# Optimization experiments

Measured on AMD Instinct MI355X. Metric: run time of the kernel, lower is better.

## Reference

```python
import jax, jax.numpy as jnp
import numpy as np

B, C, H, W = 4, 64, 128, 128
NUM_HEAD = 1
SCALE = (C // NUM_HEAD) ** (-0.5)


def setup_inputs():
    key = jax.random.key(0)
    ks = jax.random.split(key, 32)
    def nrm(k, shape, s=0.05):
        return jax.random.normal(k, shape, jnp.float32) * s
    inp = {"x": jax.random.normal(ks[0], (B, C, H, W), jnp.float32)}
    i = 1
    for wn, bn in [("Wq", "bq"), ("Wk", "bk"), ("Wv", "bv"), ("Wl", "bl"), ("Wo", "bo"), ("Wp", "bp")]:
        inp[wn] = nrm(ks[i], (C, C)); i += 1
        inp[bn] = nrm(ks[i], (C,)); i += 1
    inp["sch_dw"] = nrm(ks[i], (C, 1, 5, 1)); i += 1
    inp["sch_dwb"] = nrm(ks[i], (C,)); i += 1
    inp["sch_pw"] = nrm(ks[i], (C, C, 1, 1)); i += 1
    inp["sch_pwb"] = nrm(ks[i], (C,)); i += 1
    inp["scv_dw"] = nrm(ks[i], (C, 1, 1, 5)); i += 1
    inp["scv_dwb"] = nrm(ks[i], (C,)); i += 1
    inp["scv_pw"] = nrm(ks[i], (C, C, 1, 1)); i += 1
    inp["scv_pwb"] = nrm(ks[i], (C,)); i += 1
    inp["convh_w"] = nrm(ks[i], (C, C, 1, 1)); i += 1
    inp["convh_b"] = nrm(ks[i], (C,)); i += 1
    inp["dsc_dw"] = nrm(ks[i], (C, 1, 3, 3)); i += 1
    inp["dsc_dwb"] = nrm(ks[i], (C,)); i += 1
    inp["dsc_pw"] = nrm(ks[i], (C, C, 1, 1)); i += 1
    inp["dsc_pwb"] = nrm(ks[i], (C,)); i += 1
    inp["ln_g"] = jnp.ones((C,), jnp.float32)
    inp["ln_b"] = jnp.zeros((C,), jnp.float32)
    return inp


def _linear(x, w, b):  # x [B,N,C], w [C,C] (torch Linear convention: y = x @ w.T + b)
    return x @ w.T + b


def _dwconv(x, w, b, pad):  # depthwise: x [B,C,H,W], w [C,1,kh,kw]
    y = jax.lax.conv_general_dilated(x, w, (1, 1), [(pad[0], pad[0]), (pad[1], pad[1])],
                                     dimension_numbers=("NCHW", "OIHW", "NCHW"),
                                     feature_group_count=x.shape[1])
    return y + b[None, :, None, None]


def _pwconv(x, w, b):  # 1x1 conv: w [Co,Ci,1,1]
    return jnp.einsum("bchw,oc->bohw", x, w[:, :, 0, 0]) + b[None, :, None, None]


def _attn(q, k, v):  # [B,N,C] each; dense NxN softmax attention
    a = jax.nn.softmax(jnp.einsum("bnc,bmc->bnm", q, k) * SCALE, axis=-1)
    return jnp.einsum("bnm,bmc->bnc", a, v)


def _up2_bilinear(x):  # bilinear, scale 2, align_corners=True
    Bb, Cc, Hh, Ww = x.shape
    def coords(n):
        s = jnp.linspace(0.0, n - 1.0, 2 * n)
        i0 = jnp.floor(s).astype(jnp.int32)
        i1 = jnp.minimum(i0 + 1, n - 1)
        return i0, i1, (s - i0).astype(x.dtype)
    y0, y1, wy = coords(Hh)
    x0, x1, wx = coords(Ww)
    r = x[:, :, y0, :] * (1.0 - wy)[None, None, :, None] + x[:, :, y1, :] * wy[None, None, :, None]
    return r[:, :, :, x0] * (1.0 - wx) + r[:, :, :, x1] * wx


def _forward(x, Wq, bq, Wk, bk, Wv, bv, Wl, bl, Wo, bo, Wp, bp,
             sch_dw, sch_dwb, sch_pw, sch_pwb, scv_dw, scv_dwb, scv_pw, scv_pwb,
             convh_w, convh_b, dsc_dw, dsc_dwb, dsc_pw, dsc_pwb, ln_g, ln_b):
    Bb, Cc, Hh, Ww = x.shape
    # AvgPool2d(2,2)
    xp = x.reshape(Bb, Cc, Hh // 2, 2, Ww // 2, 2).mean((3, 5))
    Hp, Wp_ = Hh // 2, Ww // 2
    N = Hp * Wp_
    # forward_lpg: GAP-gated self-attention producing low-freq prompt
    gap = xp.mean((2, 3), keepdims=True)
    xg = (gap * xp).reshape(Bb, Cc, N).transpose(0, 2, 1)  # [B,N,C]
    q = _linear(xg, Wq, bq); k = _linear(xg, Wk, bk); v = _linear(xg, Wv, bv)
    prompt_l = _linear(_attn(q, k, v), Wl, bl).transpose(0, 2, 1).reshape(Bb, Cc, Hp, Wp_)
    # forward_hpg: separable strip-conv branches -> high-freq prompt
    x_h = _pwconv(jax.nn.gelu(_dwconv(xp, sch_dw, sch_dwb, (2, 0)), approximate=False), sch_pw, sch_pwb)
    x_v = _pwconv(jax.nn.gelu(_dwconv(xp, scv_dw, scv_dwb, (0, 2)), approximate=False), scv_pw, scv_pwb)
    prompt_h = _pwconv(x_h + x_v, convh_w, convh_b)
    # forward_pgc: cross-attention Q=high, K=low, V=linear(x)
    x_V = _linear(xp.reshape(Bb, Cc, N).transpose(0, 2, 1), Wo, bo)
    x_K = prompt_l.reshape(Bb, Cc, N).transpose(0, 2, 1)
    x_Q = prompt_h.reshape(Bb, Cc, N).transpose(0, 2, 1)
    prompt = _attn(x_Q, x_K, x_V)
    prompt = _linear(prompt, Wp, bp) + x_V
    # LayerNorm over channel dim
    mu = prompt.mean(-1, keepdims=True)
    var = jnp.mean((prompt - mu) ** 2, axis=-1, keepdims=True)
    p_norm = (prompt - mu) / jnp.sqrt(var + 1e-5) * ln_g + ln_b
    p_norm = p_norm.transpose(0, 2, 1).reshape(Bb, Cc, Hp, Wp_)
    # dsc: depthwise 3x3 -> GELU -> 1x1, residual
    out = _pwconv(jax.nn.gelu(_dwconv(p_norm, dsc_dw, dsc_dwb, (1, 1)), approximate=False), dsc_pw, dsc_pwb) + p_norm
    return _up2_bilinear(out)


def reference(x, Wq, bq, Wk, bk, Wv, bv, Wl, bl, Wo, bo, Wp, bp,
              sch_dw, sch_dwb, sch_pw, sch_pwb, scv_dw, scv_dwb, scv_pw, scv_pwb,
              convh_w, convh_b, dsc_dw, dsc_dwb, dsc_pw, dsc_pwb, ln_g, ln_b):
    return _forward(x, Wq, bq, Wk, bk, Wv, bv, Wl, bl, Wo, bo, Wp, bp,
                    sch_dw, sch_dwb, sch_pw, sch_pwb, scv_dw, scv_dwb, scv_pw, scv_pwb,
                    convh_w, convh_b, dsc_dw, dsc_dwb, dsc_pw, dsc_pwb, ln_g, ln_b)
```

## Files before the change

### kernel.cpp

```cpp
#include <hip/hip_runtime.h>
#include <math.h>

#define Bn 4
#define Cn 64
#define Np 4096
#define NSPLIT 4
#define SCALE2 0.18033688011112042f

typedef unsigned short ushort_t;
typedef __attribute__((ext_vector_type(4))) float f32x4;
typedef __attribute__((ext_vector_type(8))) short bf16x8;
typedef __attribute__((ext_vector_type(4))) short bf16x4;

__device__ __forceinline__ float gelu_exact(float x) {
    return 0.5f * x * (1.0f + erff(x * 0.70710678118654752440f));
}
__device__ __forceinline__ ushort_t f2bf(float f) {
    unsigned int u = __float_as_uint(f);
    u += 0x7fffu + ((u >> 16) & 1u);
    return (ushort_t)(u >> 16);
}
__device__ __forceinline__ ushort_t f2bf_tr(float f) {
    return (ushort_t)(__float_as_uint(f) >> 16);
}
__device__ __forceinline__ float bf2f(ushort_t h) {
    return __uint_as_float(((unsigned int)h) << 16);
}
__device__ __forceinline__ void gload_lds16(const ushort_t* g, ushort_t* l) {
    __builtin_amdgcn_global_load_lds(
        (const __attribute__((address_space(1))) void*)g,
        (__attribute__((address_space(3))) void*)l, 16, 0, 0);
}
__device__ __forceinline__ bf16x8 cvt8(const float v[8]) {
    bf16x8 r;
    #pragma unroll
    for (int j = 0; j < 8; ++j) r[j] = (short)f2bf(v[j]);
    return r;
}
__device__ __forceinline__ void gemm16(const bf16x8 af[2], const float* __restrict__ W,
                                       int l16, int quad, f32x4* acc) {
    #pragma unroll
    for (int cb = 0; cb < 4; ++cb) {
        #pragma unroll
        for (int ks = 0; ks < 2; ++ks) {
            const float* p = W + (cb * 16 + l16) * 64 + ks * 32 + quad * 8;
            float v[8];
            #pragma unroll
            for (int j = 0; j < 8; ++j) v[j] = p[j];
            acc[cb] = __builtin_amdgcn_mfma_f32_16x16x32_bf16(af[ks], cvt8(v), acc[cb], 0, 0, 0);
        }
    }
}
__device__ __forceinline__ void gemm16T(const bf16x8 af[2], const float* __restrict__ W,
                                        int l16, int quad, f32x4* acc) {
    #pragma unroll
    for (int cb = 0; cb < 4; ++cb) {
        #pragma unroll
        for (int ks = 0; ks < 2; ++ks) {
            const float* p = W + (cb * 16 + l16) * 64 + ks * 32 + quad * 8;
            float v[8];
            #pragma unroll
            for (int j = 0; j < 8; ++j) v[j] = p[j];
            acc[cb] = __builtin_amdgcn_mfma_f32_16x16x32_bf16(cvt8(v), af[ks], acc[cb], 0, 0, 0);
        }
    }
}
__device__ __forceinline__ void aload(const float* xs, int row, int quad, bf16x8 af[2]) {
    #pragma unroll
    for (int ks = 0; ks < 2; ++ks) {
        float v[8];
        #pragma unroll
        for (int j = 0; j < 8; ++j) v[j] = xs[(ks * 32 + quad * 8 + j) * 65 + row];
        af[ks] = cvt8(v);
    }
}
__device__ __forceinline__ void stage_bchw(const float* __restrict__ X, int b, int n0, int t,
                                           float* xs) {
    #pragma unroll
    for (int u = 0; u < 16; ++u) {
        int idx = t + u * 256;
        int c = idx >> 6, nl = idx & 63;
        xs[c * 65 + nl] = X[((size_t)(b * Cn + c)) * Np + n0 + nl];
    }
}
__device__ __forceinline__ void stage_comb(const ushort_t* __restrict__ OpB, const float* linv,
                                           int b, int n0, int t, float* xs) {
    const size_t SS = (size_t)Bn * Np * Cn;
    #pragma unroll
    for (int u = 0; u < 16; ++u) {
        int idx = t + u * 256;
        int nl = idx >> 6, c = idx & 63;
        size_t gi = ((size_t)(b * Np + n0 + nl)) * Cn + c;
        float s = bf2f(OpB[gi]) + bf2f(OpB[SS + gi]) +
                  bf2f(OpB[2 * SS + gi]) + bf2f(OpB[3 * SS + gi]);
        xs[c * 65 + nl] = s * linv[nl];
    }
}
__device__ __forceinline__ void store_bnc_T(ushort_t* __restrict__ Y, int b, int n, int quad,
                                            const f32x4* acc, const float* __restrict__ bias,
                                            float mult) {
    #pragma unroll
    for (int cb = 0; cb < 4; ++cb) {
        int o0 = cb * 16 + quad * 4;
        ushort4 pk;
        pk.x = f2bf((acc[cb][0] + bias[o0 + 0]) * mult);
        pk.y = f2bf((acc[cb][1] + bias[o0 + 1]) * mult);
        pk.z = f2bf((acc[cb][2] + bias[o0 + 2]) * mult);
        pk.w = f2bf((acc[cb][3] + bias[o0 + 3]) * mult);
        *(ushort4*)(Y + ((size_t)(b * Np + n)) * Cn + o0) = pk;
    }
}
__device__ __forceinline__ void store_bchw_bf16(ushort_t* __restrict__ Y, int b, int nb, int l16,
                                                const f32x4* acc, const float* __restrict__ bias) {
    #pragma unroll
    for (int cb = 0; cb < 4; ++cb) {
        int col = cb * 16 + l16;
        float bb = bias[col];
        ushort4 pk;
        pk.x = f2bf(acc[cb][0] + bb); pk.y = f2bf(acc[cb][1] + bb);
        pk.z = f2bf(acc[cb][2] + bb); pk.w = f2bf(acc[cb][3] + bb);
        *(ushort4*)(Y + ((size_t)(b * Cn + col)) * Np + nb) = pk;
    }
}

__global__ void avgpool_kernel(const float* __restrict__ x, float* __restrict__ xp,
                               float* __restrict__ gap4k,
                               const float* __restrict__ convh_w, const float* __restrict__ convh_b,
                               const float* __restrict__ sch_pw, const float* __restrict__ sch_pwb,
                               const float* __restrict__ scv_pw, const float* __restrict__ scv_pwb,
                               float* __restrict__ Wc1, float* __restrict__ Wc2,
                               float* __restrict__ bcv) {
    if (blockIdx.x < 4096) {
        int idx = blockIdx.x * 256 + threadIdx.x;
        int j  = idx & 63;
        int i  = (idx >> 6) & 63;
        int bc = idx >> 12;
        const float* p = x + ((size_t)bc * 128 + 2 * i) * 128 + 2 * j;
        float v = 0.25f * (p[0] + p[1] + p[128] + p[129]);
        xp[idx] = v;
        float s = v;
        #pragma unroll
        for (int off = 1; off < 64; off <<= 1) s += __shfl_xor(s, off, 64);
        __shared__ float sm[4];
        if ((threadIdx.x & 63) == 0) sm[threadIdx.x >> 6] = s;
        __syncthreads();
        if (threadIdx.x == 0) gap4k[blockIdx.x] = sm[0] + sm[1] + sm[2] + sm[3];
    } else {
        int g = (blockIdx.x - 4096) * 256 + threadIdx.x;
        int sel = g >> 12, idx = g & 4095;
        int o = idx >> 6, c = idx & 63;
        const float* pw = sel ? scv_pw : sch_pw;
        float acc = 0.f;
        #pragma unroll 8
        for (int m = 0; m < 64; ++m) acc += convh_w[o * 64 + m] * pw[m * 64 + c];
        (sel ? Wc2 : Wc1)[idx] = acc * SCALE2;
        if (g < 64) {
            float ab = convh_b[g];
            for (int m = 0; m < 64; ++m) ab += convh_w[g * 64 + m] * (sch_pwb[m] + scv_pwb[m]);
            bcv[g] = ab * SCALE2;
        }
    }
}

__global__ __launch_bounds__(256) void qkv_dw_kernel(
    const float* __restrict__ xp, const float* __restrict__ gap4k,
    const float* __restrict__ Wq, const float* __restrict__ bq,
    const float* __restrict__ Wk, const float* __restrict__ bk,
    const float* __restrict__ Wv, const float* __restrict__ bv,
    const float* __restrict__ Wo, const float* __restrict__ bo,
    ushort_t* __restrict__ qb, ushort_t* __restrict__ kb, ushort_t* __restrict__ vb,
    float* __restrict__ xV, ushort_t* __restrict__ xVtb,
    const float* __restrict__ wv5, const float* __restrict__ bv5,
    const float* __restrict__ wh5, const float* __restrict__ bh5,
    ushort_t* __restrict__ gh, ushort_t* __restrict__ gv) {
    int b = blockIdx.y, t = threadIdx.x;
    if (blockIdx.x >= 64) {
        int part = blockIdx.x - 64;
        int e = part * 1024 + t * 4;
        size_t base = (size_t)b * (Cn * Np) + e;
        int c = e >> 12, i = (e >> 6) & 63, j = e & 63;
        const float* p = xp + ((size_t)(b * Cn + c)) * Np;
        float accV[4], accH[4];
        #pragma unroll
        for (int k = 0; k < 4; ++k) { accV[k] = bv5[c]; accH[k] = bh5[c]; }
        #pragma unroll
        for (int d = 0; d < 5; ++d) {
            int ii = i + d - 2;
            if (ii >= 0 && ii < 64) {
                #pragma unroll
                for (int k = 0; k < 4; ++k) accV[k] += wv5[c * 5 + d] * p[ii * 64 + j + k];
            }
        }
        #pragma unroll
        for (int k = 0; k < 4; ++k) {
            #pragma unroll
            for (int d = 0; d < 5; ++d) {
                int jj = j + k + d - 2;
                if (jj >= 0 && jj < 64) accH[k] += wh5[c * 5 + d] * p[i * 64 + jj];
            }
        }
        ushort4 ph, pv_;
        ph.x = f2bf(gelu_exact(accV[0])); ph.y = f2bf(gelu_exact(accV[1]));
        ph.z = f2bf(gelu_exact(accV[2])); ph.w = f2bf(gelu_exact(accV[3]));
        pv_.x = f2bf(gelu_exact(accH[0])); pv_.y = f2bf(gelu_exact(accH[1]));
        pv_.z = f2bf(gelu_exact(accH[2])); pv_.w = f2bf(gelu_exact(accH[3]));
        *(ushort4*)(gh + base) = ph;
        *(ushort4*)(gv + base) = pv_;
        return;
    }
    __shared__ float xs[64 * 65];
    __shared__ float gl[64];
    int n0 = blockIdx.x * 64;
    int wv_ = t >> 6, lane = t & 63, l16 = lane & 15, quad = lane >> 4;
    stage_bchw(xp, b, n0, t, xs);
    if (t < 64) {
        float s = 0.f;
        #pragma unroll
        for (int u = 0; u < 16; ++u) s += gap4k[(b * 64 + t) * 16 + u];
        gl[t] = s * (1.f / 4096.f);
    }
    __syncthreads();
    int row = wv_ * 16 + l16;
    int n   = n0 + wv_ * 16 + l16;
    int nb  = n0 + wv_ * 16 + quad * 4;
    bf16x8 ar[2], ag[2];
    #pragma unroll
    for (int ks = 0; ks < 2; ++ks) {
        float vr[8], vg[8];
        #pragma unroll
        for (int j = 0; j < 8; ++j) {
            int k = ks * 32 + quad * 8 + j;
            float xv = xs[k * 65 + row];
            vr[j] = xv; vg[j] = xv * gl[k];
        }
        ar[ks] = cvt8(vr); ag[ks] = cvt8(vg);
    }
    f32x4 acc[4];
    #pragma unroll
    for (int cb = 0; cb < 4; ++cb) acc[cb] = (f32x4){0.f, 0.f, 0.f, 0.f};
    gemm16T(ag, Wq, l16, quad, acc);
    store_bnc_T(qb, b, n, quad, acc, bq, SCALE2);
    #pragma unroll
    for (int cb = 0; cb < 4; ++cb) acc[cb] = (f32x4){0.f, 0.f, 0.f, 0.f};
    gemm16T(ag, Wk, l16, quad, acc);
    store_bnc_T(kb, b, n, quad, acc, bk, 1.f);
    #pragma unroll
    for (int cb = 0; cb < 4; ++cb) acc[cb] = (f32x4){0.f, 0.f, 0.f, 0.f};
    gemm16(ag, Wv, l16, quad, acc);
    store_bchw_bf16(vb, b, nb, l16, acc, bv);
    #pragma unroll
    for (int cb = 0; cb < 4; ++cb) acc[cb] = (f32x4){0.f, 0.f, 0.f, 0.f};
    gemm16(ar, Wo, l16, quad, acc);
    #pragma unroll
    for (int cb = 0; cb < 4; ++cb) {
        int col = cb * 16 + l16;
        float bb = bo[col];
        ushort4 pk;
        float y0 = acc[cb][0] + bb, y1 = acc[cb][1] + bb, y2 = acc[cb][2] + bb, y3 = acc[cb][3] + bb;
        xV[((size_t)(b * Np + nb + 0)) * Cn + col] = y0;
        xV[((size_t)(b * Np + nb + 1)) * Cn + col] = y1;
        xV[((size_t)(b * Np + nb + 2)) * Cn + col] = y2;
        xV[((size_t)(b * Np + nb + 3)) * Cn + col] = y3;
        pk.x = f2bf(y0); pk.y = f2bf(y1); pk.z = f2bf(y2); pk.w = f2bf(y3);
        *(ushort4*)(xVtb + ((size_t)(b * Cn + col)) * Np + nb) = pk;
    }
}

__device__ __forceinline__ void attn_body(
    int xblk, int b, const ushort_t* __restrict__ Qb, const ushort_t* __restrict__ Kb,
    const ushort_t* __restrict__ Vtb, ushort_t* __restrict__ OpB, float* __restrict__ Lpart,
    ushort_t* smem) {
    ushort_t* kt0 = smem;
    ushort_t* vt0 = smem + 8192;
    int split = xblk >> 6;
    int qt    = xblk & 63;
    int n0    = qt * 64;
    int t     = threadIdx.x;
    int wave  = t >> 6, lane = t & 63;
    int l16   = lane & 15, quad = lane >> 4;

    const ushort_t* qp = Qb + ((size_t)(b * Np) + n0 + wave * 16 + l16) * Cn + quad * 8;
    bf16x8 aq0 = *(const bf16x8*)(qp);
    bf16x8 aq1 = *(const bf16x8*)(qp + 32);

    f32x4 oa[4];
    float psum = 0.f;
    #pragma unroll
    for (int db = 0; db < 4; ++db) oa[db] = (f32x4){0.f, 0.f, 0.f, 0.f};

    int lrow = lane >> 3;
    int kvbase = split * (Np / NSPLIT);
    const ushort_t* Kg = Qb == nullptr ? nullptr : Kb + ((size_t)b * Np) * Cn;
    const ushort_t* Vg = Vtb + ((size_t)b * Cn) * Np;

    auto stage = [&](int buf, int k0) {
        int wh = wave & 1;
        if (wave < 2) {
            ushort_t* dst = kt0 + buf * 4096 + wh * 2048;
            #pragma unroll
            for (int u = 0; u < 4; ++u) {
                int r = wh * 32 + u * 8 + lrow;
                int jsw = ((lane & 7) ^ lrow ^ (wh * 4 + u)) & 7;
                gload_lds16(Kg + ((size_t)(k0 + r)) * Cn + jsw * 8, dst + u * 512);
            }
        } else {
            ushort_t* dst = vt0 + buf * 4096 + wh * 2048;
            #pragma unroll
            for (int u = 0; u < 4; ++u) {
                int d = wh * 32 + u * 8 + lrow;
                int jsw = ((lane & 7) ^ lrow ^ (wh * 4 + u)) & 7;
                gload_lds16(Vg + (size_t)d * Np + k0 + jsw * 8, dst + u * 512);
            }
        }
    };
    const int NT = (Np / NSPLIT) / 64;
    stage(0, kvbase);
    __syncthreads();

    for (int m = 0; m < NT; ++m) {
        int cur = m & 1;
        if (m + 1 < NT) stage(1 - cur, kvbase + (m + 1) * 64);
        const ushort_t* ktc = kt0 + cur * 4096;
        const ushort_t* vtc = vt0 + cur * 4096;

        f32x4 sa[4];
        #pragma unroll
        for (int cb = 0; cb < 4; ++cb) sa[cb] = (f32x4){0.f, 0.f, 0.f, 0.f};
        #pragma unroll
        for (int cb = 0; cb < 4; ++cb) {
            int key = ((l16 & 7) ^ (cb * 2 + (l16 >> 3))) & 7;
            const ushort_t* krow = ktc + (cb * 16 + l16) * 64;
            bf16x8 bk0 = *(const bf16x8*)(krow + ((quad    ) ^ key) * 8);
            bf16x8 bk1 = *(const bf16x8*)(krow + ((quad + 4) ^ key) * 8);
            sa[cb] = __builtin_amdgcn_mfma_f32_16x16x32_bf16(bk0, aq0, sa[cb], 0, 0, 0);
            sa[cb] = __builtin_amdgcn_mfma_f32_16x16x32_bf16(bk1, aq1, sa[cb], 0, 0, 0);
        }
        bf16x4 pb[4];
        #pragma unroll
        for (int cb = 0; cb < 4; ++cb) {
            float p0 = exp2f(sa[cb][0]), p1 = exp2f(sa[cb][1]);
            float p2 = exp2f(sa[cb][2]), p3 = exp2f(sa[cb][3]);
            psum += (p0 + p1) + (p2 + p3);
            bf16x4 pk;
            pk[0] = (short)f2bf_tr(p0); pk[1] = (short)f2bf_tr(p1);
            pk[2] = (short)f2bf_tr(p2); pk[3] = (short)f2bf_tr(p3);
            pb[cb] = pk;
        }
        #pragma unroll
        for (int kc = 0; kc < 4; ++kc) {
            #pragma unroll
            for (int db = 0; db < 4; ++db) {
                int d = db * 16 + l16;
                int key = ((l16 & 7) ^ (db * 2 + (l16 >> 3))) & 7;
                int phys = (kc * 2 + (quad >> 1)) ^ key;
                const ushort_t* va = vtc + d * 64 + phys * 8 + (quad & 1) * 4;
                bf16x4 av = *(const bf16x4*)va;
                oa[db] = __builtin_amdgcn_mfma_f32_16x16x16bf16_1k(av, pb[kc], oa[db], 0, 0, 0);
            }
        }
        __syncthreads();
    }
    psum += __shfl_xor(psum, 16, 64);
    psum += __shfl_xor(psum, 32, 64);
    size_t obase = ((size_t)(split * Bn + b)) * Np;
    int n = n0 + wave * 16 + l16;
    if (quad == 0) Lpart[obase + n] = psum;
    #pragma unroll
    for (int db = 0; db < 4; ++db) {
        ushort4 pk;
        pk.x = f2bf(oa[db][0]); pk.y = f2bf(oa[db][1]);
        pk.z = f2bf(oa[db][2]); pk.w = f2bf(oa[db][3]);
        *(ushort4*)(OpB + (obase + n) * Cn + db * 16 + quad * 4) = pk;
    }
}

__device__ __forceinline__ void hpg_body(
    int tile, int b, const ushort_t* __restrict__ gh, const ushort_t* __restrict__ gv,
    const float* __restrict__ Wc1, const float* __restrict__ Wc2, const float* __restrict__ bcv,
    ushort_t* __restrict__ xQb, ushort_t* smem) {
    ushort_t* xs1 = smem;
    ushort_t* xs2 = smem + 4608;
    int n0 = tile * 64, t = threadIdx.x;
    int wv_ = t >> 6, lane = t & 63, l16 = lane & 15, quad = lane >> 4;
    #pragma unroll
    for (int u = 0; u < 4; ++u) {
        int lin = u * 256 + t;
        int c = lin >> 4, nl4 = (lin & 15) * 4;
        size_t gi = ((size_t)(b * Cn + c)) * Np + n0 + nl4;
        ushort4 g1 = *(const ushort4*)(gh + gi);
        ushort4 g2 = *(const ushort4*)(gv + gi);
        xs1[(nl4 + 0) * 72 + c] = g1.x; xs1[(nl4 + 1) * 72 + c] = g1.y;
        xs1[(nl4 + 2) * 72 + c] = g1.z; xs1[(nl4 + 3) * 72 + c] = g1.w;
        xs2[(nl4 + 0) * 72 + c] = g2.x; xs2[(nl4 + 1) * 72 + c] = g2.y;
        xs2[(nl4 + 2) * 72 + c] = g2.z; xs2[(nl4 + 3) * 72 + c] = g2.w;
    }
    __syncthreads();
    int row = wv_ * 16 + l16;
    bf16x8 a1[2], a2[2];
    #pragma unroll
    for (int ks = 0; ks < 2; ++ks) {
        a1[ks] = *(const bf16x8*)(xs1 + row * 72 + ks * 32 + quad * 8);
        a2[ks] = *(const bf16x8*)(xs2 + row * 72 + ks * 32 + quad * 8);
    }
    f32x4 acc[4];
    #pragma unroll
    for (int cb = 0; cb < 4; ++cb) acc[cb] = (f32x4){0.f, 0.f, 0.f, 0.f};
    gemm16T(a1, Wc1, l16, quad, acc);
    gemm16T(a2, Wc2, l16, quad, acc);
    store_bnc_T(xQb, b, n0 + wv_ * 16 + l16, quad, acc, bcv, 1.f);
}

__global__ __launch_bounds__(256) void attn_hpg_kernel(
    const ushort_t* __restrict__ Qb, const ushort_t* __restrict__ Kb,
    const ushort_t* __restrict__ Vtb, ushort_t* __restrict__ OpB, float* __restrict__ Lpart,
    const ushort_t* __restrict__ gh, const ushort_t* __restrict__ gv,
    const float* __restrict__ Wc1, const float* __restrict__ Wc2,
    const float* __restrict__ bcv, ushort_t* __restrict__ xQb) {
    __shared__ ushort_t smem[16384];
    int b = blockIdx.y;
    if (blockIdx.x < 256)
        attn_body(blockIdx.x, b, Qb, Kb, Vtb, OpB, Lpart, smem);
    else
        hpg_body(blockIdx.x - 256, b, gh, gv, Wc1, Wc2, bcv, xQb, smem);
}

__global__ __launch_bounds__(256) void wl_mfma(
    const ushort_t* __restrict__ OpB, const float* __restrict__ Lp,
    const float* __restrict__ Wl, const float* __restrict__ bl, ushort_t* __restrict__ xKb) {
    __shared__ float xs[64 * 65];
    __shared__ float linv[64];
    int b = blockIdx.y, n0 = blockIdx.x * 64, t = threadIdx.x;
    int wv_ = t >> 6, lane = t & 63, l16 = lane & 15, quad = lane >> 4;
    if (t < 64) {
        size_t li = (size_t)b * Np + n0 + t;
        const size_t LS = (size_t)Bn * Np;
        linv[t] = 1.f / (Lp[li] + Lp[LS + li] + Lp[2 * LS + li] + Lp[3 * LS + li]);
    }
    __syncthreads();
    stage_comb(OpB, linv, b, n0, t, xs);
    __syncthreads();
    bf16x8 af[2];
    aload(xs, wv_ * 16 + l16, quad, af);
    f32x4 acc[4];
    #pragma unroll
    for (int cb = 0; cb < 4; ++cb) acc[cb] = (f32x4){0.f, 0.f, 0.f, 0.f};
    gemm16T(af, Wl, l16, quad, acc);
    store_bnc_T(xKb, b, n0 + wv_ * 16 + l16, quad, acc, bl, 1.f);
}

__global__ __launch_bounds__(256) void linln_mfma(
    const ushort_t* __restrict__ OpB, const float* __restrict__ Lp,
    const float* __restrict__ Wp, const float* __restrict__ bp,
    const float* __restrict__ xV, const float* __restrict__ g, const float* __restrict__ beta,
    float* __restrict__ out) {
    __shared__ float xs[64 * 65];
    __shared__ float linv[64];
    int b = blockIdx.y, n0 = blockIdx.x * 64, t = threadIdx.x;
    int wv_ = t >> 6, lane = t & 63, l16 = lane & 15, quad = lane >> 4;
    if (t < 64) {
        size_t li = (size_t)b * Np + n0 + t;
        const size_t LS = (size_t)Bn * Np;
        linv[t] = 1.f / (Lp[li] + Lp[LS + li] + Lp[2 * LS + li] + Lp[3 * LS + li]);
    }
    __syncthreads();
    stage_comb(OpB, linv, b, n0, t, xs);
    __syncthreads();
    bf16x8 af[2];
    aload(xs, wv_ * 16 + l16, quad, af);
    f32x4 acc[4];
    #pragma unroll
    for (int cb = 0; cb < 4; ++cb) acc[cb] = (f32x4){0.f, 0.f, 0.f, 0.f};
    gemm16(af, Wp, l16, quad, acc);
    int nb = n0 + wv_ * 16 + quad * 4;
    float vals[4][4], gc[4], bec[4];
    #pragma unroll
    for (int cb = 0; cb < 4; ++cb) {
        int col = cb * 16 + l16;
        float bb = bp[col];
        gc[cb] = g[col]; bec[cb] = beta[col];
        #pragma unroll
        for (int r = 0; r < 4; ++r)
            vals[cb][r] = acc[cb][r] + bb + xV[((size_t)(b * Np + nb + r)) * Cn + col];
    }
    f32x4 yn[4];
    #pragma unroll
    for (int r = 0; r < 4; ++r) {
        float s = 0.f, s2 = 0.f;
        #pragma unroll
        for (int cb = 0; cb < 4; ++cb) { s += vals[cb][r]; s2 += vals[cb][r] * vals[cb][r]; }
        #pragma unroll
        for (int off = 1; off < 16; off <<= 1) {
            s  += __shfl_xor(s, off, 64);
            s2 += __shfl_xor(s2, off, 64);
        }
        float mu  = s * (1.f / 64.f);
        float var = s2 * (1.f / 64.f) - mu * mu;
        float ivs = rsqrtf(var + 1e-5f);
        #pragma unroll
        for (int cb = 0; cb < 4; ++cb)
            yn[cb][r] = (vals[cb][r] - mu) * ivs * gc[cb] + bec[cb];
    }
    #pragma unroll
    for (int cb = 0; cb < 4; ++cb)
        *(f32x4*)(out + ((size_t)(b * Cn + cb * 16 + l16)) * Np + nb) = yn[cb];
}

__global__ void dw3x3_gelu_kernel(const float* __restrict__ xin, const float* __restrict__ w,
                                  const float* __restrict__ bias, float* __restrict__ out) {
    int idx = blockIdx.x * 256 + threadIdx.x;
    int j = idx & 63, i = (idx >> 6) & 63, bc = idx >> 12, c = bc & 63;
    const float* p = xin + (size_t)bc * Np;
    float acc = bias[c];
    #pragma unroll
    for (int dy = 0; dy < 3; ++dy) {
        int ii = i + dy - 1;
        if (ii < 0 || ii >= 64) continue;
        #pragma unroll
        for (int dx = 0; dx < 3; ++dx) {
            int jj = j + dx - 1;
            if (jj < 0 || jj >= 64) continue;
            acc += w[c * 9 + dy * 3 + dx] * p[ii * 64 + jj];
        }
    }
    out[idx] = gelu_exact(acc);
}

__global__ __launch_bounds__(256) void dsc_mfma(
    const float* __restrict__ X, const float* __restrict__ W, const float* __restrict__ bias,
    const float* __restrict__ res, float* __restrict__ out) {
    __shared__ float xs[64 * 65];
    int b = blockIdx.y, n0 = blockIdx.x * 64, t = threadIdx.x;
    int wv_ = t >> 6, lane = t & 63, l16 = lane & 15, quad = lane >> 4;
    stage_bchw(X, b, n0, t, xs);
    __syncthreads();
    bf16x8 af[2];
    aload(xs, wv_ * 16 + l16, quad, af);
    f32x4 acc[4];
    #pragma unroll
    for (int cb = 0; cb < 4; ++cb) acc[cb] = (f32x4){0.f, 0.f, 0.f, 0.f};
    gemm16(af, W, l16, quad, acc);
    int nb = n0 + wv_ * 16 + quad * 4;
    #pragma unroll
    for (int cb = 0; cb < 4; ++cb) {
        int col = cb * 16 + l16;
        float bb = bias[col];
        size_t oi = ((size_t)(b * Cn + col)) * Np + nb;
        f32x4 rv = *(const f32x4*)(res + oi);
        f32x4 v4;
        #pragma unroll
        for (int r = 0; r < 4; ++r) v4[r] = acc[cb][r] + bb + rv[r];
        *(f32x4*)(out + oi) = v4;
    }
}

__global__ void upsample_kernel(const float* __restrict__ in, float* __restrict__ out) {
    int idx = blockIdx.x * 256 + threadIdx.x;
    int x  = idx & 127;
    int y  = (idx >> 7) & 127;
    int bc = idx >> 14;
    float sy = y * (63.f / 127.f);
    float sx = x * (63.f / 127.f);
    int y0 = (int)sy, x0 = (int)sx;
    float fy = sy - y0, fx = sx - x0;
    int y1 = min(y0 + 1, 63), x1 = min(x0 + 1, 63);
    const float* p = in + (size_t)bc * Np;
    float v00 = p[y0 * 64 + x0], v01 = p[y0 * 64 + x1];
    float v10 = p[y1 * 64 + x0], v11 = p[y1 * 64 + x1];
    out[idx] = (v00 * (1.f - fx) + v01 * fx) * (1.f - fy) +
               (v10 * (1.f - fx) + v11 * fx) * fy;
}

extern "C" void kernel_launch(void* const* d_in, const int* in_sizes, int n_in,
                              void* d_out, int out_size, void* d_ws, size_t ws_size,
                              hipStream_t stream) {
    const float* x       = (const float*)d_in[0];
    const float* Wq      = (const float*)d_in[1];
    const float* bq      = (const float*)d_in[2];
    const float* Wk      = (const float*)d_in[3];
    const float* bk      = (const float*)d_in[4];
    const float* Wv      = (const float*)d_in[5];
    const float* bv      = (const float*)d_in[6];
    const float* Wl      = (const float*)d_in[7];
    const float* bl      = (const float*)d_in[8];
    const float* Wo      = (const float*)d_in[9];
    const float* bo      = (const float*)d_in[10];
    const float* Wp      = (const float*)d_in[11];
    const float* bp      = (const float*)d_in[12];
    const float* sch_dw  = (const float*)d_in[13];
    const float* sch_dwb = (const float*)d_in[14];
    const float* sch_pw  = (const float*)d_in[15];
    const float* sch_pwb = (const float*)d_in[16];
    const float* scv_dw  = (const float*)d_in[17];
    const float* scv_dwb = (const float*)d_in[18];
    const float* scv_pw  = (const float*)d_in[19];
    const float* scv_pwb = (const float*)d_in[20];
    const float* convh_w = (const float*)d_in[21];
    const float* convh_b = (const float*)d_in[22];
    const float* dsc_dw  = (const float*)d_in[23];
    const float* dsc_dwb = (const float*)d_in[24];
    const float* dsc_pw  = (const float*)d_in[25];
    const float* dsc_pwb = (const float*)d_in[26];
    const float* ln_g    = (const float*)d_in[27];
    const float* ln_b    = (const float*)d_in[28];

    float* ws = (float*)d_ws;
    const size_t SZ = (size_t)Bn * Np * Cn;
    float* xp   = ws;
    float* xV   = ws + SZ;
    ushort_t* ghb = (ushort_t*)(ws + 2 * SZ);
    ushort_t* gh  = ghb;
    ushort_t* gv  = ghb + SZ;
    float* f2   = ws + 2 * SZ;
    ushort_t* bws  = (ushort_t*)(ws + 3 * SZ);
    ushort_t* qb   = bws;
    ushort_t* kb_  = bws + SZ;
    ushort_t* vb   = bws + 2 * SZ;
    ushort_t* xKb  = bws + 3 * SZ;
    ushort_t* xVtb = bws + 4 * SZ;
    ushort_t* xQb  = bws + 5 * SZ;
    ushort_t* OpB  = (ushort_t*)(ws + 6 * SZ);
    float* gap4k  = ws + 8 * SZ;
    float* Lpart  = gap4k + 4096;
    float* Wc1  = Lpart + (size_t)NSPLIT * Bn * Np;
    float* Wc2  = Wc1 + 4096;
    float* bcv  = Wc2 + 4096;

    dim3 g64(64, Bn);

    avgpool_kernel<<<4096 + 32, 256, 0, stream>>>(x, xp, gap4k,
                                                  convh_w, convh_b, sch_pw, sch_pwb,
                                                  scv_pw, scv_pwb, Wc1, Wc2, bcv);
    qkv_dw_kernel<<<dim3(64 + 256, Bn), 256, 0, stream>>>(
        xp, gap4k, Wq, bq, Wk, bk, Wv, bv, Wo, bo,
        qb, kb_, vb, xV, xVtb, sch_dw, sch_dwb, scv_dw, scv_dwb, gh, gv);
    attn_hpg_kernel<<<dim3(256 + 64, Bn), 256, 0, stream>>>(
        qb, kb_, vb, OpB, Lpart, gh, gv, Wc1, Wc2, bcv, xQb);
    wl_mfma<<<g64, 256, 0, stream>>>(OpB, Lpart, Wl, bl, xKb);
    attn_hpg_kernel<<<dim3(256, Bn), 256, 0, stream>>>(
        xQb, xKb, xVtb, OpB, Lpart, gh, gv, Wc1, Wc2, bcv, xQb);
    linln_mfma<<<g64, 256, 0, stream>>>(OpB, Lpart, Wp, bp, xV, ln_g, ln_b, xp);
    dw3x3_gelu_kernel<<<4096, 256, 0, stream>>>(xp, dsc_dw, dsc_dwb, xV);
    dsc_mfma<<<g64, 256, 0, stream>>>(xV, dsc_pw, dsc_pwb, xp, f2);
    upsample_kernel<<<16384, 256, 0, stream>>>(f2, (float*)d_out);
}
```

Measured before the change: 245.4 us.

## Pre-convert weights to bf16 once and vectorize staging, dwconv and upsample loads

All 64x64 weight matrices are converted to bf16 once, in extra blocks of the first kernel, so the MFMA GEMMs load packed bf16x8 operands instead of eight floats each followed by per-element conversion. The OpB partial combine now reads ushort4 vectors, the depthwise 5-tap convolutions use float4 row loads with a register window, and the bilinear upsample writes four outputs per thread with a float4 store. Together these cut redundant weight conversion and scalar global accesses, at the cost of a slightly larger first launch and scattered LDS writes in stage_comb.

```diff
diff --git a/kernel.cpp b/kernel.cpp
--- a/kernel.cpp
+++ b/kernel.cpp
@@ -37,31 +37,25 @@
     for (int j = 0; j < 8; ++j) r[j] = (short)f2bf(v[j]);
     return r;
 }
-__device__ __forceinline__ void gemm16(const bf16x8 af[2], const float* __restrict__ W,
-                                       int l16, int quad, f32x4* acc) {
+__device__ __forceinline__ void gemm16b(const bf16x8 af[2], const ushort_t* __restrict__ Wb,
+                                        int l16, int quad, f32x4* acc) {
     #pragma unroll
     for (int cb = 0; cb < 4; ++cb) {
         #pragma unroll
         for (int ks = 0; ks < 2; ++ks) {
-            const float* p = W + (cb * 16 + l16) * 64 + ks * 32 + quad * 8;
-            float v[8];
-            #pragma unroll
-            for (int j = 0; j < 8; ++j) v[j] = p[j];
-            acc[cb] = __builtin_amdgcn_mfma_f32_16x16x32_bf16(af[ks], cvt8(v), acc[cb], 0, 0, 0);
-        }
-    }
-}
-__device__ __forceinline__ void gemm16T(const bf16x8 af[2], const float* __restrict__ W,
-                                        int l16, int quad, f32x4* acc) {
+            bf16x8 bw = *(const bf16x8*)(Wb + (cb * 16 + l16) * 64 + ks * 32 + quad * 8);
+            acc[cb] = __builtin_amdgcn_mfma_f32_16x16x32_bf16(af[ks], bw, acc[cb], 0, 0, 0);
+        }
+    }
+}
+__device__ __forceinline__ void gemm16Tb(const bf16x8 af[2], const ushort_t* __restrict__ Wb,
+                                         int l16, int quad, f32x4* acc) {
     #pragma unroll
     for (int cb = 0; cb < 4; ++cb) {
         #pragma unroll
         for (int ks = 0; ks < 2; ++ks) {
-            const float* p = W + (cb * 16 + l16) * 64 + ks * 32 + quad * 8;
-            float v[8];
-            #pragma unroll
-            for (int j = 0; j < 8; ++j) v[j] = p[j];
-            acc[cb] = __builtin_amdgcn_mfma_f32_16x16x32_bf16(cvt8(v), af[ks], acc[cb], 0, 0, 0);
+            bf16x8 bw = *(const bf16x8*)(Wb + (cb * 16 + l16) * 64 + ks * 32 + quad * 8);
+            acc[cb] = __builtin_amdgcn_mfma_f32_16x16x32_bf16(bw, af[ks], acc[cb], 0, 0, 0);
         }
     }
 }
@@ -86,14 +80,20 @@
 __device__ __forceinline__ void stage_comb(const ushort_t* __restrict__ OpB, const float* linv,
                                            int b, int n0, int t, float* xs) {
     const size_t SS = (size_t)Bn * Np * Cn;
-    #pragma unroll
-    for (int u = 0; u < 16; ++u) {
-        int idx = t + u * 256;
-        int nl = idx >> 6, c = idx & 63;
-        size_t gi = ((size_t)(b * Np + n0 + nl)) * Cn + c;
-        float s = bf2f(OpB[gi]) + bf2f(OpB[SS + gi]) +
-                  bf2f(OpB[2 * SS + gi]) + bf2f(OpB[3 * SS + gi]);
-        xs[c * 65 + nl] = s * linv[nl];
+    int c4 = (t & 15) * 4;
+    #pragma unroll
+    for (int u = 0; u < 4; ++u) {
+        int nl = (t >> 4) + u * 16;
+        size_t gi = ((size_t)(b * Np + n0 + nl)) * Cn + c4;
+        ushort4 a0 = *(const ushort4*)(OpB + gi);
+        ushort4 a1 = *(const ushort4*)(OpB + SS + gi);
+        ushort4 a2 = *(const ushort4*)(OpB + 2 * SS + gi);
+        ushort4 a3 = *(const ushort4*)(OpB + 3 * SS + gi);
+        float li = linv[nl];
+        xs[(c4 + 0) * 65 + nl] = (bf2f(a0.x) + bf2f(a1.x) + bf2f(a2.x) + bf2f(a3.x)) * li;
+        xs[(c4 + 1) * 65 + nl] = (bf2f(a0.y) + bf2f(a1.y) + bf2f(a2.y) + bf2f(a3.y)) * li;
+        xs[(c4 + 2) * 65 + nl] = (bf2f(a0.z) + bf2f(a1.z) + bf2f(a2.z) + bf2f(a3.z)) * li;
+        xs[(c4 + 3) * 65 + nl] = (bf2f(a0.w) + bf2f(a1.w) + bf2f(a2.w) + bf2f(a3.w)) * li;
     }
 }
 __device__ __forceinline__ void store_bnc_T(ushort_t* __restrict__ Y, int b, int n, int quad,
@@ -128,8 +128,12 @@
                                const float* __restrict__ convh_w, const float* __restrict__ convh_b,
                                const float* __restrict__ sch_pw, const float* __restrict__ sch_pwb,
                                const float* __restrict__ scv_pw, const float* __restrict__ scv_pwb,
-                               float* __restrict__ Wc1, float* __restrict__ Wc2,
-                               float* __restrict__ bcv) {
+                               ushort_t* __restrict__ Wc1b, ushort_t* __restrict__ Wc2b,
+                               float* __restrict__ bcv,
+                               const float* __restrict__ Wq, const float* __restrict__ Wk,
+                               const float* __restrict__ Wv, const float* __restrict__ Wo,
+                               const float* __restrict__ Wl, const float* __restrict__ Wp,
+                               const float* __restrict__ dscpw, ushort_t* __restrict__ Wball) {
     if (blockIdx.x < 4096) {
         int idx = blockIdx.x * 256 + threadIdx.x;
         int j  = idx & 63;
@@ -145,7 +149,7 @@
         if ((threadIdx.x & 63) == 0) sm[threadIdx.x >> 6] = s;
         __syncthreads();
         if (threadIdx.x == 0) gap4k[blockIdx.x] = sm[0] + sm[1] + sm[2] + sm[3];
-    } else {
+    } else if (blockIdx.x < 4128) {
         int g = (blockIdx.x - 4096) * 256 + threadIdx.x;
         int sel = g >> 12, idx = g & 4095;
         int o = idx >> 6, c = idx & 63;
@@ -153,21 +157,26 @@
         float acc = 0.f;
         #pragma unroll 8
         for (int m = 0; m < 64; ++m) acc += convh_w[o * 64 + m] * pw[m * 64 + c];
-        (sel ? Wc2 : Wc1)[idx] = acc * SCALE2;
+        (sel ? Wc2b : Wc1b)[idx] = f2bf(acc * SCALE2);
         if (g < 64) {
             float ab = convh_b[g];
             for (int m = 0; m < 64; ++m) ab += convh_w[g * 64 + m] * (sch_pwb[m] + scv_pwb[m]);
             bcv[g] = ab * SCALE2;
         }
+    } else {
+        int g = (blockIdx.x - 4128) * 256 + threadIdx.x;
+        int which = g >> 12, idx = g & 4095;
+        const float* srcs[7] = {Wq, Wk, Wv, Wo, Wl, Wp, dscpw};
+        Wball[g] = f2bf(srcs[which][idx]);
     }
 }
 
 __global__ __launch_bounds__(256) void qkv_dw_kernel(
     const float* __restrict__ xp, const float* __restrict__ gap4k,
-    const float* __restrict__ Wq, const float* __restrict__ bq,
-    const float* __restrict__ Wk, const float* __restrict__ bk,
-    const float* __restrict__ Wv, const float* __restrict__ bv,
-    const float* __restrict__ Wo, const float* __restrict__ bo,
+    const ushort_t* __restrict__ Wqb, const float* __restrict__ bq,
+    const ushort_t* __restrict__ Wkb, const float* __restrict__ bk,
+    const ushort_t* __restrict__ Wvb, const float* __restrict__ bv,
+    const ushort_t* __restrict__ Wob, const float* __restrict__ bo,
     ushort_t* __restrict__ qb, ushort_t* __restrict__ kb, ushort_t* __restrict__ vb,
     float* __restrict__ xV, ushort_t* __restrict__ xVtb,
     const float* __restrict__ wv5, const float* __restrict__ bv5,
@@ -187,17 +196,23 @@
         for (int d = 0; d < 5; ++d) {
             int ii = i + d - 2;
             if (ii >= 0 && ii < 64) {
-                #pragma unroll
-                for (int k = 0; k < 4; ++k) accV[k] += wv5[c * 5 + d] * p[ii * 64 + j + k];
+                f32x4 r = *(const f32x4*)(p + ii * 64 + j);
+                float w = wv5[c * 5 + d];
+                accV[0] += w * r[0]; accV[1] += w * r[1];
+                accV[2] += w * r[2]; accV[3] += w * r[3];
             }
         }
+        f32x4 c0 = *(const f32x4*)(p + i * 64 + j);
+        float col[8];
+        col[2] = c0[0]; col[3] = c0[1]; col[4] = c0[2]; col[5] = c0[3];
+        col[0] = (j >= 2)     ? p[i * 64 + j - 2] : 0.f;
+        col[1] = (j >= 1)     ? p[i * 64 + j - 1] : 0.f;
+        col[6] = (j + 4 < 64) ? p[i * 64 + j + 4] : 0.f;
+        col[7] = (j + 5 < 64) ? p[i * 64 + j + 5] : 0.f;
         #pragma unroll
         for (int k = 0; k < 4; ++k) {
             #pragma unroll
-            for (int d = 0; d < 5; ++d) {
-                int jj = j + k + d - 2;
-                if (jj >= 0 && jj < 64) accH[k] += wh5[c * 5 + d] * p[i * 64 + jj];
-            }
+            for (int d = 0; d < 5; ++d) accH[k] += wh5[c * 5 + d] * col[k + d];
         }
         ushort4 ph, pv_;
         ph.x = f2bf(gelu_exact(accV[0])); ph.y = f2bf(gelu_exact(accV[1]));
@@ -238,19 +253,19 @@
     f32x4 acc[4];
     #pragma unroll
     for (int cb = 0; cb < 4; ++cb) acc[cb] = (f32x4){0.f, 0.f, 0.f, 0.f};
-    gemm16T(ag, Wq, l16, quad, acc);
+    gemm16Tb(ag, Wqb, l16, quad, acc);
     store_bnc_T(qb, b, n, quad, acc, bq, SCALE2);
     #pragma unroll
     for (int cb = 0; cb < 4; ++cb) acc[cb] = (f32x4){0.f, 0.f, 0.f, 0.f};
-    gemm16T(ag, Wk, l16, quad, acc);
+    gemm16Tb(ag, Wkb, l16, quad, acc);
     store_bnc_T(kb, b, n, quad, acc, bk, 1.f);
     #pragma unroll
     for (int cb = 0; cb < 4; ++cb) acc[cb] = (f32x4){0.f, 0.f, 0.f, 0.f};
-    gemm16(ag, Wv, l16, quad, acc);
+    gemm16b(ag, Wvb, l16, quad, acc);
     store_bchw_bf16(vb, b, nb, l16, acc, bv);
     #pragma unroll
     for (int cb = 0; cb < 4; ++cb) acc[cb] = (f32x4){0.f, 0.f, 0.f, 0.f};
-    gemm16(ar, Wo, l16, quad, acc);
+    gemm16b(ar, Wob, l16, quad, acc);
     #pragma unroll
     for (int cb = 0; cb < 4; ++cb) {
         int col = cb * 16 + l16;
@@ -376,7 +391,8 @@
 
 __device__ __forceinline__ void hpg_body(
     int tile, int b, const ushort_t* __restrict__ gh, const ushort_t* __restrict__ gv,
-    const float* __restrict__ Wc1, const float* __restrict__ Wc2, const float* __restrict__ bcv,
+    const ushort_t* __restrict__ Wc1b, const ushort_t* __restrict__ Wc2b,
+    const float* __restrict__ bcv,
     ushort_t* __restrict__ xQb, ushort_t* smem) {
     ushort_t* xs1 = smem;
     ushort_t* xs2 = smem + 4608;
@@ -405,8 +421,8 @@
     f32x4 acc[4];
     #pragma unroll
     for (int cb = 0; cb < 4; ++cb) acc[cb] = (f32x4){0.f, 0.f, 0.f, 0.f};
-    gemm16T(a1, Wc1, l16, quad, acc);
-    gemm16T(a2, Wc2, l16, quad, acc);
+    gemm16Tb(a1, Wc1b, l16, quad, acc);
+    gemm16Tb(a2, Wc2b, l16, quad, acc);
     store_bnc_T(xQb, b, n0 + wv_ * 16 + l16, quad, acc, bcv, 1.f);
 }
 
@@ -414,19 +430,19 @@
     const ushort_t* __restrict__ Qb, const ushort_t* __restrict__ Kb,
     const ushort_t* __restrict__ Vtb, ushort_t* __restrict__ OpB, float* __restrict__ Lpart,
     const ushort_t* __restrict__ gh, const ushort_t* __restrict__ gv,
-    const float* __restrict__ Wc1, const float* __restrict__ Wc2,
+    const ushort_t* __restrict__ Wc1b, const ushort_t* __restrict__ Wc2b,
     const float* __restrict__ bcv, ushort_t* __restrict__ xQb) {
     __shared__ ushort_t smem[16384];
     int b = blockIdx.y;
     if (blockIdx.x < 256)
         attn_body(blockIdx.x, b, Qb, Kb, Vtb, OpB, Lpart, smem);
     else
-        hpg_body(blockIdx.x - 256, b, gh, gv, Wc1, Wc2, bcv, xQb, smem);
+        hpg_body(blockIdx.x - 256, b, gh, gv, Wc1b, Wc2b, bcv, xQb, smem);
 }
 
 __global__ __launch_bounds__(256) void wl_mfma(
     const ushort_t* __restrict__ OpB, const float* __restrict__ Lp,
-    const float* __restrict__ Wl, const float* __restrict__ bl, ushort_t* __restrict__ xKb) {
+    const ushort_t* __restrict__ Wlb, const float* __restrict__ bl, ushort_t* __restrict__ xKb) {
     __shared__ float xs[64 * 65];
     __shared__ float linv[64];
     int b = blockIdx.y, n0 = blockIdx.x * 64, t = threadIdx.x;
@@ -444,13 +460,13 @@
     f32x4 acc[4];
     #pragma unroll
     for (int cb = 0; cb < 4; ++cb) acc[cb] = (f32x4){0.f, 0.f, 0.f, 0.f};
-    gemm16T(af, Wl, l16, quad, acc);
+    gemm16Tb(af, Wlb, l16, quad, acc);
     store_bnc_T(xKb, b, n0 + wv_ * 16 + l16, quad, acc, bl, 1.f);
 }
 
 __global__ __launch_bounds__(256) void linln_mfma(
     const ushort_t* __restrict__ OpB, const float* __restrict__ Lp,
-    const float* __restrict__ Wp, const float* __restrict__ bp,
+    const ushort_t* __restrict__ Wpb, const float* __restrict__ bp,
     const float* __restrict__ xV, const float* __restrict__ g, const float* __restrict__ beta,
     float* __restrict__ out) {
     __shared__ float xs[64 * 65];
@@ -470,7 +486,7 @@
     f32x4 acc[4];
     #pragma unroll
     for (int cb = 0; cb < 4; ++cb) acc[cb] = (f32x4){0.f, 0.f, 0.f, 0.f};
-    gemm16(af, Wp, l16, quad, acc);
+    gemm16b(af, Wpb, l16, quad, acc);
     int nb = n0 + wv_ * 16 + quad * 4;
     float vals[4][4], gc[4], bec[4];
     #pragma unroll
@@ -526,7 +542,7 @@
 }
 
 __global__ __launch_bounds__(256) void dsc_mfma(
-    const float* __restrict__ X, const float* __restrict__ W, const float* __restrict__ bias,
+    const float* __restrict__ X, const ushort_t* __restrict__ Wb, const float* __restrict__ bias,
     const float* __restrict__ res, float* __restrict__ out) {
     __shared__ float xs[64 * 65];
     int b = blockIdx.y, n0 = blockIdx.x * 64, t = threadIdx.x;
@@ -538,7 +554,7 @@
     f32x4 acc[4];
     #pragma unroll
     for (int cb = 0; cb < 4; ++cb) acc[cb] = (f32x4){0.f, 0.f, 0.f, 0.f};
-    gemm16(af, W, l16, quad, acc);
+    gemm16b(af, Wb, l16, quad, acc);
     int nb = n0 + wv_ * 16 + quad * 4;
     #pragma unroll
     for (int cb = 0; cb < 4; ++cb) {
@@ -555,19 +571,28 @@
 
 __global__ void upsample_kernel(const float* __restrict__ in, float* __restrict__ out) {
     int idx = blockIdx.x * 256 + threadIdx.x;
-    int x  = idx & 127;
-    int y  = (idx >> 7) & 127;
-    int bc = idx >> 14;
+    int x4 = (idx & 31) * 4;
+    int y  = (idx >> 5) & 127;
+    int bc = idx >> 12;
     float sy = y * (63.f / 127.f);
-    float sx = x * (63.f / 127.f);
-    int y0 = (int)sy, x0 = (int)sx;
-    float fy = sy - y0, fx = sx - x0;
-    int y1 = min(y0 + 1, 63), x1 = min(x0 + 1, 63);
-    const float* p = in + (size_t)bc * Np;
-    float v00 = p[y0 * 64 + x0], v01 = p[y0 * 64 + x1];
-    float v10 = p[y1 * 64 + x0], v11 = p[y1 * 64 + x1];
-    out[idx] = (v00 * (1.f - fx) + v01 * fx) * (1.f - fy) +
-               (v10 * (1.f - fx) + v11 * fx) * fy;
+    int y0 = (int)sy;
+    float fy = sy - y0;
+    int y1 = min(y0 + 1, 63);
+    const float* p0 = in + (size_t)bc * Np + y0 * 64;
+    const float* p1 = in + (size_t)bc * Np + y1 * 64;
+    f32x4 o;
+    #pragma unroll
+    for (int k = 0; k < 4; ++k) {
+        int xo = x4 + k;
+        float sx = xo * (63.f / 127.f);
+        int x0 = (int)sx;
+        float fx = sx - x0;
+        int x1 = min(x0 + 1, 63);
+        float r0 = p0[x0] + (p0[x1] - p0[x0]) * fx;
+        float r1 = p1[x0] + (p1[x1] - p1[x0]) * fx;
+        o[k] = r0 + (r1 - r0) * fy;
+    }
+    *(f32x4*)(out + (size_t)idx * 4) = o;
 }
 
 extern "C" void kernel_launch(void* const* d_in, const int* in_sizes, int n_in,
@@ -621,25 +646,35 @@
     ushort_t* OpB  = (ushort_t*)(ws + 6 * SZ);
     float* gap4k  = ws + 8 * SZ;
     float* Lpart  = gap4k + 4096;
-    float* Wc1  = Lpart + (size_t)NSPLIT * Bn * Np;
-    float* Wc2  = Wc1 + 4096;
-    float* bcv  = Wc2 + 4096;
+    float* wcslot = Lpart + (size_t)NSPLIT * Bn * Np;
+    ushort_t* Wc1b = (ushort_t*)wcslot;
+    ushort_t* Wc2b = Wc1b + 4096;
+    float* bcv  = wcslot + 4096;
+    ushort_t* Wball = (ushort_t*)(bcv + 64);
+    ushort_t* Wqb   = Wball;
+    ushort_t* Wkb   = Wball + 4096;
+    ushort_t* Wvb   = Wball + 8192;
+    ushort_t* Wob   = Wball + 12288;
+    ushort_t* Wlb   = Wball + 16384;
+    ushort_t* Wpb   = Wball + 20480;
+    ushort_t* Wdscb = Wball + 24576;
 
     dim3 g64(64, Bn);
 
-    avgpool_kernel<<<4096 + 32, 256, 0, stream>>>(x, xp, gap4k,
+    avgpool_kernel<<<4096 + 32 + 112, 256, 0, stream>>>(x, xp, gap4k,
                                                   convh_w, convh_b, sch_pw, sch_pwb,
-                                                  scv_pw, scv_pwb, Wc1, Wc2, bcv);
+                                                  scv_pw, scv_pwb, Wc1b, Wc2b, bcv,
+                                                  Wq, Wk, Wv, Wo, Wl, Wp, dsc_pw, Wball);
     qkv_dw_kernel<<<dim3(64 + 256, Bn), 256, 0, stream>>>(
-        xp, gap4k, Wq, bq, Wk, bk, Wv, bv, Wo, bo,
+        xp, gap4k, Wqb, bq, Wkb, bk, Wvb, bv, Wob, bo,
         qb, kb_, vb, xV, xVtb, sch_dw, sch_dwb, scv_dw, scv_dwb, gh, gv);
     attn_hpg_kernel<<<dim3(256 + 64, Bn), 256, 0, stream>>>(
-        qb, kb_, vb, OpB, Lpart, gh, gv, Wc1, Wc2, bcv, xQb);
-    wl_mfma<<<g64, 256, 0, stream>>>(OpB, Lpart, Wl, bl, xKb);
+        qb, kb_, vb, OpB, Lpart, gh, gv, Wc1b, Wc2b, bcv, xQb);
+    wl_mfma<<<g64, 256, 0, stream>>>(OpB, Lpart, Wlb, bl, xKb);
     attn_hpg_kernel<<<dim3(256, Bn), 256, 0, stream>>>(
-        xQb, xKb, xVtb, OpB, Lpart, gh, gv, Wc1, Wc2, bcv, xQb);
-    linln_mfma<<<g64, 256, 0, stream>>>(OpB, Lpart, Wp, bp, xV, ln_g, ln_b, xp);
+        xQb, xKb, xVtb, OpB, Lpart, gh, gv, Wc1b, Wc2b, bcv, xQb);
+    linln_mfma<<<g64, 256, 0, stream>>>(OpB, Lpart, Wpb, bp, xV, ln_g, ln_b, xp);
     dw3x3_gelu_kernel<<<4096, 256, 0, stream>>>(xp, dsc_dw, dsc_dwb, xV);
-    dsc_mfma<<<g64, 256, 0, stream>>>(xV, dsc_pw, dsc_pwb, xp, f2);
-    upsample_kernel<<<16384, 256, 0, stream>>>(f2, (float*)d_out);
-}
+    dsc_mfma<<<g64, 256, 0, stream>>>(xV, Wdscb, dsc_pwb, xp, f2);
+    upsample_kernel<<<4096, 256, 0, stream>>>(f2, (float*)d_out);
+}
```

Result: no change. 242.0 us (-1.4%).
